# Kernel optimization log

Measured on AMD Instinct MI355X. Metric: run time of the kernel, lower is better.

The kernel has to match this reference:

```python
import jax, jax.numpy as jnp
import numpy as np

B, SX, SY, D = 32, 2048, 2048, 160

def setup_inputs() -> dict:
    key = jax.random.key(0)
    ks = jax.random.split(key, 5)
    s = 1.0 / np.sqrt(D)
    return {
        "x": jax.random.normal(ks[0], (B, SX, D), dtype=jnp.float32),
        "y": jax.random.normal(ks[1], (B, SY, D), dtype=jnp.float32),
        "Wq": jax.random.normal(ks[2], (D, D), dtype=jnp.float32) * s,
        "bq": jnp.zeros((D,), dtype=jnp.float32),
        "Wk": jax.random.normal(ks[3], (D, D), dtype=jnp.float32) * s,
        "bk": jnp.zeros((D,), dtype=jnp.float32),
        "Wv": jax.random.normal(ks[4], (D, D), dtype=jnp.float32) * s,
        "bv": jnp.zeros((D,), dtype=jnp.float32),
    }

def reference(x, y, Wq, bq, Wk, bk, Wv, bv):
    # torch nn.Linear: out = in @ W.T + b, W is [out_dim, in_dim]
    q = jnp.einsum('bxd,ed->bxe', x, Wq) + bq          # [B,SX,D]
    k = jnp.einsum('byd,ed->bye', y, Wk) + bk          # [B,SY,D]
    v = jnp.einsum('byd,ed->bye', y, Wv) + bv          # [B,SY,D]
    scores = jnp.einsum('bxd,byd->bxy', q, k)          # [B,SX,SY] (no scaling in source)
    attn = jax.nn.softmax(scores, axis=-1)
    out = jnp.einsum('bxy,byd->bxd', attn, v)          # dropout is identity at eval
    return out + x                                     # residual
```

## Files before the change

### kernel.cpp

```cpp
#include <hip/hip_runtime.h>

#define LOG2E 1.44269504088896340736f

typedef _Float16 f16;
typedef __attribute__((ext_vector_type(2))) _Float16 f16x2;
typedef __attribute__((ext_vector_type(2))) __fp16 fp16x2;
typedef __attribute__((ext_vector_type(4))) _Float16 f16x4;
typedef __attribute__((ext_vector_type(8))) _Float16 f16x8;
typedef __attribute__((ext_vector_type(4))) float f32x4;
typedef __attribute__((ext_vector_type(16))) float f32x16;
typedef __attribute__((ext_vector_type(8))) unsigned short us8;
typedef __attribute__((ext_vector_type(2))) int i32x2;

#define BB 32
#define SSX 2048
#define SSY 2048
#define DD 160
#define M_TOTAL (BB*SSX)

#define PRS 168
#define VTRS 136
#define RS 168
#define KVB 32
#define VRS 40

__device__ __forceinline__ f32x4 mfma16(f16x8 a, f16x8 b, f32x4 c) {
  return __builtin_amdgcn_mfma_f32_16x16x32_f16(a, b, c, 0, 0, 0);
}

__device__ __forceinline__ f32x16 mfma32(f16x8 a, f16x8 b, f32x16 c) {
  return __builtin_amdgcn_mfma_f32_32x32x16_f16(a, b, c, 0, 0, 0);
}

__device__ __forceinline__ unsigned pk2rtz(float a, float b) {
  union { fp16x2 h; unsigned u; } x;
  x.h = __builtin_amdgcn_cvt_pkrtz(a, b);
  return x.u;
}

__global__ __launch_bounds__(256) void wcvt_kernel(
    const float* __restrict__ Wq, const float* __restrict__ Wk, const float* __restrict__ Wv,
    f16* __restrict__ Wf)
{
  int idx = blockIdx.x*256 + threadIdx.x;
  int which = idx / 6400;
  int off   = idx % 6400;
  const float* src = (which == 0) ? Wq : (which == 1 ? Wk : Wv);
  float4 v = *(const float4*)&src[off*4];
  f16x4 h = { (f16)v.x, (f16)v.y, (f16)v.z, (f16)v.w };
  *(f16x4*)&Wf[which*25600 + off*4] = h;
}

__global__ __launch_bounds__(256, 3) void proj_kernel(
    const float* __restrict__ x, const float* __restrict__ y,
    const float* __restrict__ bq, const float* __restrict__ bk, const float* __restrict__ bv,
    const f16* __restrict__ Wf,
    f16* __restrict__ Qw, f16* __restrict__ Kw, f16* __restrict__ Vtw)
{
  __shared__ __align__(16) f16 buf[160*PRS];
  const int t = threadIdx.x;
  const int wave = t >> 6;
  const int lane = t & 63;
  const int quad = lane >> 4;
  const int l16  = lane & 15;
  const int bid  = (blockIdx.x & 7) * 192 + (blockIdx.x >> 3);
  const int kind = bid % 3;
  const int tile = bid / 3;
  const int row0 = tile * 128;
  const float* src  = (kind == 0) ? x  : y;
  const f16*   W    = Wf + kind*25600;
  const float* bias = (kind == 0) ? bq : (kind == 1 ? bk : bv);

  #pragma unroll
  for (int i = 0; i < 12; ++i) {
    int idx = t + i*256;
    int r = idx / 20, g = idx % 20;
    *(us8*)&buf[r*PRS + g*8] = *(const us8*)&W[idx*8];
  }
  if (t < 128) {
    int idx = t + 3072;
    int r = idx / 20, g = idx % 20;
    *(us8*)&buf[r*PRS + g*8] = *(const us8*)&W[idx*8];
  }

  f16x8 afr0[5], afr1[5];
  {
    const float* r0p = src + (size_t)(row0 + wave*32 + l16)*DD;
    const float* r1p = r0p + 16*DD;
    #pragma unroll
    for (int ks = 0; ks < 5; ++ks) {
      float4 a = *(const float4*)&r0p[ks*32 + quad*8];
      float4 b = *(const float4*)&r0p[ks*32 + quad*8 + 4];
      afr0[ks] = (f16x8){(f16)a.x,(f16)a.y,(f16)a.z,(f16)a.w,
                         (f16)b.x,(f16)b.y,(f16)b.z,(f16)b.w};
      float4 c = *(const float4*)&r1p[ks*32 + quad*8];
      float4 d = *(const float4*)&r1p[ks*32 + quad*8 + 4];
      afr1[ks] = (f16x8){(f16)c.x,(f16)c.y,(f16)c.z,(f16)c.w,
                         (f16)d.x,(f16)d.y,(f16)d.z,(f16)d.w};
    }
  }
  __syncthreads();

  f32x4 acc0[10], acc1[10];
  #pragma unroll
  for (int nt = 0; nt < 10; ++nt) {
    float bs = bias[nt*16 + l16];
    acc0[nt] = (f32x4){bs,bs,bs,bs};
    acc1[nt] = (f32x4){bs,bs,bs,bs};
    #pragma unroll
    for (int ks = 0; ks < 5; ++ks) {
      f16x8 bfr = *(const f16x8*)&buf[(nt*16 + l16)*PRS + ks*32 + quad*8];
      acc0[nt] = mfma16(afr0[ks], bfr, acc0[nt]);
      acc1[nt] = mfma16(afr1[ks], bfr, acc1[nt]);
    }
  }
  __syncthreads();

  if (kind < 2) {
    f16* dst = (kind == 0) ? Qw : Kw;
    #pragma unroll
    for (int nt = 0; nt < 10; ++nt)
      #pragma unroll
      for (int r = 0; r < 4; ++r) {
        buf[(wave*32 + quad*4 + r)*PRS + nt*16 + l16]      = (f16)acc0[nt][r];
        buf[(wave*32 + 16 + quad*4 + r)*PRS + nt*16 + l16] = (f16)acc1[nt][r];
      }
    __syncthreads();
    for (int i = 0; i < 10; ++i) {
      int idx = t + i*256;
      int r = idx / 20, g = idx % 20;
      *(us8*)&dst[(size_t)(row0 + r)*DD + g*8] = *(const us8*)&buf[r*PRS + g*8];
    }
  } else {
    #pragma unroll
    for (int nt = 0; nt < 10; ++nt)
      #pragma unroll
      for (int r = 0; r < 4; ++r) {
        buf[(nt*16 + l16)*VTRS + wave*32 + quad*4 + r]      = (f16)acc0[nt][r];
        buf[(nt*16 + l16)*VTRS + wave*32 + 16 + quad*4 + r] = (f16)acc1[nt][r];
      }
    __syncthreads();
    const int b  = row0 / SSY;
    const int y0 = row0 % SSY;
    for (int i = 0; i < 10; ++i) {
      int idx = t + i*256;
      int d = idx / 16, yg = idx % 16;
      *(us8*)&Vtw[((size_t)b*DD + d)*SSY + y0 + yg*8] = *(const us8*)&buf[d*VTRS + yg*8];
    }
  }
}


#define LOAD_CHUNK(yb) { \
  const f16* ksrc = Kw + ((size_t)b*SSY + (yb))*DD; \
  const f16* vsrc = Vtw + (size_t)b*DD*SSY + (yb); \
  _Pragma("unroll") \
  for (int i = 0; i < 5; ++i) { \
    int idx = t + i*128; int r = idx/20, c = idx%20; \
    kreg[i] = *(const us8*)&ksrc[(size_t)r*DD + c*8]; \
  } \
  _Pragma("unroll") \
  for (int i = 0; i < 5; ++i) { \
    int idx = t + i*128; int d = idx>>2, g = idx&3; \
    vreg[i] = *(const us8*)&vsrc[(size_t)d*SSY + g*8]; \
  } \
}

#define STORE_CHUNK() { \
  _Pragma("unroll") \
  for (int i = 0; i < 5; ++i) { \
    int idx = t + i*128; int r = idx/20, c = idx%20; \
    *(us8*)&K_lds[r*RS + c*8] = kreg[i]; \
  } \
  _Pragma("unroll") \
  for (int i = 0; i < 5; ++i) { \
    int idx = t + i*128; int d = idx>>2, g = idx&3; \
    *(us8*)&Vt_lds[d*VRS + g*8] = vreg[i]; \
  } \
}

__global__ __launch_bounds__(128, 2) void flash_kernel(
    const f16* __restrict__ Qw, const f16* __restrict__ Kw, const f16* __restrict__ Vtw,
    const float* __restrict__ x, float* __restrict__ out)
{
  __shared__ __align__(16) f16 K_lds[KVB*RS];
  __shared__ __align__(16) f16 Vt_lds[160*VRS];
  const int t = threadIdx.x;
  const int wave = t >> 6;
  const int lane = t & 63;
  const int l31  = lane & 31;
  const int hi   = lane >> 5;
  const int bid  = (blockIdx.x & 7) * 128 + (blockIdx.x >> 3);
  const int b    = bid >> 5;
  const int x0   = (bid & 31) * 64;

  us8 kreg[5], vreg[5];
  LOAD_CHUNK(0);

  f16x8 qfr[10];
  #pragma unroll
  for (int h = 0; h < 2; ++h) {
    if (h) __syncthreads();
    const f16* qsrc = Qw + ((size_t)b*SSX + x0 + h*32)*DD;
    for (int i = 0; i < 5; ++i) {
      int idx = t + i*128;
      int r = idx / 20, c = idx % 20;
      *(us8*)&K_lds[r*RS + c*8] = *(const us8*)&qsrc[(size_t)r*DD + c*8];
    }
    __syncthreads();
    if (wave == h) {
      #pragma unroll
      for (int s = 0; s < 10; ++s)
        qfr[s] = *(const f16x8*)&K_lds[l31*RS + s*16 + hi*8];
    }
  }

  f32x16 acc[5];
  #pragma unroll
  for (int i = 0; i < 5; ++i)
    #pragma unroll
    for (int r = 0; r < 16; ++r) acc[i][r] = 0.f;
  float m = -1e30f, l = 0.f;

  for (int yc = 0; yc < SSY/KVB; ++yc) {
    __syncthreads();
    STORE_CHUNK();
    __syncthreads();
    if (yc < SSY/KVB - 1) LOAD_CHUNK((yc+1)*KVB);

    f32x16 S0;
    #pragma unroll
    for (int r = 0; r < 16; ++r) S0[r] = 0.f;
    __builtin_amdgcn_s_setprio(1);
    #pragma unroll
    for (int s = 0; s < 10; ++s) {
      f16x8 k0 = *(const f16x8*)&K_lds[l31*RS + s*16 + hi*8];
      S0 = mfma32(k0, qfr[s], S0);
    }
    __builtin_amdgcn_s_setprio(0);

    float pmax = fmaxf(S0[0], S0[1]);
    #pragma unroll
    for (int r = 2; r < 16; r += 2) pmax = fmaxf(fmaxf(pmax, S0[r]), S0[r+1]);
    pmax = fmaxf(pmax, __shfl_xor(pmax, 32));

    if (__any(pmax > m + 8.f)) {
      float n  = fmaxf(m, pmax);
      float sc = exp2f((m - n)*LOG2E);
      m = n; l *= sc;
      #pragma unroll
      for (int r = 0; r < 16; ++r) {
        float scq = __shfl(sc, (r&3) + 8*(r>>2) + 4*hi);
        #pragma unroll
        for (int dt = 0; dt < 5; ++dt) acc[dt][r] *= scq;
      }
    }

    float lsum = 0.f;
    #pragma unroll
    for (int r = 0; r < 16; ++r) { S0[r] = exp2f((S0[r] - m)*LOG2E); lsum += S0[r]; }
    lsum += __shfl_xor(lsum, 32);
    l += lsum;

    #pragma unroll
    for (int c = 0; c < 2; ++c) {
      const int bo = c*8;
      unsigned L0 = pk2rtz(S0[bo+0], S0[bo+1]), L1 = pk2rtz(S0[bo+2], S0[bo+3]);
      unsigned H0 = pk2rtz(S0[bo+4], S0[bo+5]), H1 = pk2rtz(S0[bo+6], S0[bo+7]);
      i32x2 r02 = __builtin_amdgcn_permlane32_swap((int)L0, (int)H0, false, false);
      i32x2 r13 = __builtin_amdgcn_permlane32_swap((int)L1, (int)H1, false, false);
      union { unsigned u[4]; f16x8 h; } ph;
      ph.u[0] = (unsigned)r02.x; ph.u[1] = (unsigned)r13.x;
      ph.u[2] = (unsigned)r02.y; ph.u[3] = (unsigned)r13.y;
      __builtin_amdgcn_s_setprio(1);
      #pragma unroll
      for (int dt = 0; dt < 5; ++dt) {
        int row = dt*32 + l31;
        f16x8 vf = *(const f16x8*)&Vt_lds[row*VRS + (c*2 + hi)*8];
        acc[dt] = mfma32(ph.h, vf, acc[dt]);
      }
      __builtin_amdgcn_s_setprio(0);
    }
  }

  #pragma unroll
  for (int r = 0; r < 16; ++r) {
    int qr = (r&3) + 8*(r>>2) + 4*hi;
    float rl = 1.f / __shfl(l, qr);
    size_t rowoff = ((size_t)b*SSX + x0 + wave*32 + qr)*DD + l31;
    #pragma unroll
    for (int dt = 0; dt < 5; ++dt) {
      size_t o = rowoff + (size_t)dt*32;
      out[o] = acc[dt][r]*rl + x[o];
    }
  }
}

extern "C" void kernel_launch(void* const* d_in, const int* in_sizes, int n_in,
                              void* d_out, int out_size, void* d_ws, size_t ws_size,
                              hipStream_t stream) {
  const float* x  = (const float*)d_in[0];
  const float* y  = (const float*)d_in[1];
  const float* Wq = (const float*)d_in[2];
  const float* bq = (const float*)d_in[3];
  const float* Wk = (const float*)d_in[4];
  const float* bk = (const float*)d_in[5];
  const float* Wv = (const float*)d_in[6];
  const float* bv = (const float*)d_in[7];

  f16* Qw  = (f16*)d_ws;
  f16* Kw  = Qw + (size_t)M_TOTAL*DD;
  f16* Vtw = Kw + (size_t)M_TOTAL*DD;
  size_t wf_off = (ws_size - 153600) & ~(size_t)255;
  f16* Wf = (f16*)((char*)d_ws + wf_off);

  wcvt_kernel<<<75, 256, 0, stream>>>(Wq, Wk, Wv, Wf);
  proj_kernel<<<1536, 256, 0, stream>>>(x, y, bq, bk, bv, Wf, Qw, Kw, Vtw);
  flash_kernel<<<1024, 128, 0, stream>>>(Qw, Kw, Vtw, x, (float*)d_out);
}
```

Baseline: 272.5 us.

## Double-buffer V tile in LDS and split QK MFMA chain into two accumulators

The V-transpose tile in LDS is now double-buffered. The next chunk's K/V store and the following global load are issued after the QK^T MFMAs and before softmax and PV, so loads overlap compute instead of sitting behind two barriers at the top of each iteration. The QK^T dot is split into two independent accumulator chains to cut MFMA dependency latency, and the max and sum reductions become trees. The projection kernel's launch-bounds occupancy hint drops from 3 to 2, and the extra LDS and registers may lower flash-kernel occupancy.

```diff
diff --git a/kernel.cpp b/kernel.cpp
--- a/kernel.cpp
+++ b/kernel.cpp
@@ -51,7 +51,7 @@
   *(f16x4*)&Wf[which*25600 + off*4] = h;
 }
 
-__global__ __launch_bounds__(256, 3) void proj_kernel(
+__global__ __launch_bounds__(256, 2) void proj_kernel(
     const float* __restrict__ x, const float* __restrict__ y,
     const float* __restrict__ bq, const float* __restrict__ bk, const float* __restrict__ bv,
     const f16* __restrict__ Wf,
@@ -166,7 +166,7 @@
   } \
 }
 
-#define STORE_CHUNK() { \
+#define STORE_CHUNK(vb) { \
   _Pragma("unroll") \
   for (int i = 0; i < 5; ++i) { \
     int idx = t + i*128; int r = idx/20, c = idx%20; \
@@ -175,7 +175,7 @@
   _Pragma("unroll") \
   for (int i = 0; i < 5; ++i) { \
     int idx = t + i*128; int d = idx>>2, g = idx&3; \
-    *(us8*)&Vt_lds[d*VRS + g*8] = vreg[i]; \
+    *(us8*)&Vt_lds[vb][d*VRS + g*8] = vreg[i]; \
   } \
 }
 
@@ -184,7 +184,7 @@
     const float* __restrict__ x, float* __restrict__ out)
 {
   __shared__ __align__(16) f16 K_lds[KVB*RS];
-  __shared__ __align__(16) f16 Vt_lds[160*VRS];
+  __shared__ __align__(16) f16 Vt_lds[2][160*VRS];
   const int t = threadIdx.x;
   const int wave = t >> 6;
   const int lane = t & 63;
@@ -214,6 +214,11 @@
         qfr[s] = *(const f16x8*)&K_lds[l31*RS + s*16 + hi*8];
     }
   }
+  __syncthreads();
+
+  STORE_CHUNK(0);
+  LOAD_CHUNK(KVB);
+  __syncthreads();
 
   f32x16 acc[5];
   #pragma unroll
@@ -223,25 +228,33 @@
   float m = -1e30f, l = 0.f;
 
   for (int yc = 0; yc < SSY/KVB; ++yc) {
-    __syncthreads();
-    STORE_CHUNK();
-    __syncthreads();
-    if (yc < SSY/KVB - 1) LOAD_CHUNK((yc+1)*KVB);
-
-    f32x16 S0;
-    #pragma unroll
-    for (int r = 0; r < 16; ++r) S0[r] = 0.f;
+    const int cur = yc & 1;
+
+    f32x16 Sa, Sb;
+    #pragma unroll
+    for (int r = 0; r < 16; ++r) { Sa[r] = 0.f; Sb[r] = 0.f; }
     __builtin_amdgcn_s_setprio(1);
     #pragma unroll
-    for (int s = 0; s < 10; ++s) {
-      f16x8 k0 = *(const f16x8*)&K_lds[l31*RS + s*16 + hi*8];
-      S0 = mfma32(k0, qfr[s], S0);
+    for (int s = 0; s < 5; ++s) {
+      f16x8 ka = *(const f16x8*)&K_lds[l31*RS + (2*s)*16 + hi*8];
+      f16x8 kb = *(const f16x8*)&K_lds[l31*RS + (2*s+1)*16 + hi*8];
+      Sa = mfma32(ka, qfr[2*s], Sa);
+      Sb = mfma32(kb, qfr[2*s+1], Sb);
     }
     __builtin_amdgcn_s_setprio(0);
-
-    float pmax = fmaxf(S0[0], S0[1]);
-    #pragma unroll
-    for (int r = 2; r < 16; r += 2) pmax = fmaxf(fmaxf(pmax, S0[r]), S0[r+1]);
+    __syncthreads();
+
+    if (yc < SSY/KVB - 1) STORE_CHUNK(cur ^ 1);
+    if (yc < SSY/KVB - 2) LOAD_CHUNK((yc+2)*KVB);
+
+    f32x16 S0 = Sa + Sb;
+
+    float t0 = fmaxf(S0[0], S0[1]),  t1 = fmaxf(S0[2], S0[3]);
+    float t2 = fmaxf(S0[4], S0[5]),  t3 = fmaxf(S0[6], S0[7]);
+    float t4 = fmaxf(S0[8], S0[9]),  t5 = fmaxf(S0[10], S0[11]);
+    float t6 = fmaxf(S0[12], S0[13]), t7 = fmaxf(S0[14], S0[15]);
+    t0 = fmaxf(t0, t1); t2 = fmaxf(t2, t3); t4 = fmaxf(t4, t5); t6 = fmaxf(t6, t7);
+    float pmax = fmaxf(fmaxf(t0, t2), fmaxf(t4, t6));
     pmax = fmaxf(pmax, __shfl_xor(pmax, 32));
 
     if (__any(pmax > m + 8.f)) {
@@ -256,11 +269,16 @@
       }
     }
 
-    float lsum = 0.f;
-    #pragma unroll
-    for (int r = 0; r < 16; ++r) { S0[r] = exp2f((S0[r] - m)*LOG2E); lsum += S0[r]; }
-    lsum += __shfl_xor(lsum, 32);
-    l += lsum;
+    #pragma unroll
+    for (int r = 0; r < 16; ++r) S0[r] = exp2f((S0[r] - m)*LOG2E);
+    {
+      float a0 = S0[0]+S0[1], a1 = S0[2]+S0[3], a2 = S0[4]+S0[5], a3 = S0[6]+S0[7];
+      float a4 = S0[8]+S0[9], a5 = S0[10]+S0[11], a6 = S0[12]+S0[13], a7 = S0[14]+S0[15];
+      a0 += a1; a2 += a3; a4 += a5; a6 += a7;
+      float lsum = (a0 + a2) + (a4 + a6);
+      lsum += __shfl_xor(lsum, 32);
+      l += lsum;
+    }
 
     #pragma unroll
     for (int c = 0; c < 2; ++c) {
@@ -276,11 +294,13 @@
       #pragma unroll
       for (int dt = 0; dt < 5; ++dt) {
         int row = dt*32 + l31;
-        f16x8 vf = *(const f16x8*)&Vt_lds[row*VRS + (c*2 + hi)*8];
+        f16x8 vf = *(const f16x8*)&Vt_lds[cur][row*VRS + (c*2 + hi)*8];
         acc[dt] = mfma32(ph.h, vf, acc[dt]);
       }
       __builtin_amdgcn_s_setprio(0);
     }
+
+    __syncthreads();
   }
 
   #pragma unroll
```

Measured after the change: 289.7 us. 1.06x slower.

## Split KV chunk across wave pairs with 512-thread blocks and merge softmax states

Applied to the files above, without the earlier changes.

Each block now handles 128 query rows with 8 waves. Waves are paired so that each wave of a pair processes half of a 64-row KV chunk, and the two partial online-softmax states (max, sum, accumulator) are merged through LDS at the end. This doubles the KV tile size and halves the number of blocks, amortizing K/V global loads and barriers over more query rows. The cost is an extra cross-wave reduction with several barriers and larger LDS use per block. Each wave's own online-softmax rescaling logic is unchanged.

```diff
diff --git a/kernel.cpp b/kernel.cpp
--- a/kernel.cpp
+++ b/kernel.cpp
@@ -21,8 +21,8 @@
 #define PRS 168
 #define VTRS 136
 #define RS 168
-#define KVB 32
-#define VRS 40
+#define KVB 64
+#define VRS 72
 
 __device__ __forceinline__ f32x4 mfma16(f16x8 a, f16x8 b, f32x4 c) {
   return __builtin_amdgcn_mfma_f32_16x16x32_f16(a, b, c, 0, 0, 0);
@@ -155,63 +155,73 @@
   const f16* ksrc = Kw + ((size_t)b*SSY + (yb))*DD; \
   const f16* vsrc = Vtw + (size_t)b*DD*SSY + (yb); \
   _Pragma("unroll") \
-  for (int i = 0; i < 5; ++i) { \
-    int idx = t + i*128; int r = idx/20, c = idx%20; \
-    kreg[i] = *(const us8*)&ksrc[(size_t)r*DD + c*8]; \
+  for (int i = 0; i < 3; ++i) { \
+    int idx = t + i*512; \
+    if (idx < 1280) { int r = idx/20, c = idx%20; \
+      kreg[i] = *(const us8*)&ksrc[(size_t)r*DD + c*8]; } \
   } \
   _Pragma("unroll") \
-  for (int i = 0; i < 5; ++i) { \
-    int idx = t + i*128; int d = idx>>2, g = idx&3; \
-    vreg[i] = *(const us8*)&vsrc[(size_t)d*SSY + g*8]; \
+  for (int i = 0; i < 3; ++i) { \
+    int idx = t + i*512; \
+    if (idx < 1280) { int d = idx>>3, g = idx&7; \
+      vreg[i] = *(const us8*)&vsrc[(size_t)d*SSY + g*8]; } \
   } \
 }
 
 #define STORE_CHUNK() { \
   _Pragma("unroll") \
-  for (int i = 0; i < 5; ++i) { \
-    int idx = t + i*128; int r = idx/20, c = idx%20; \
-    *(us8*)&K_lds[r*RS + c*8] = kreg[i]; \
+  for (int i = 0; i < 3; ++i) { \
+    int idx = t + i*512; \
+    if (idx < 1280) { int r = idx/20, c = idx%20; \
+      *(us8*)&K_lds[r*RS + c*8] = kreg[i]; } \
   } \
   _Pragma("unroll") \
-  for (int i = 0; i < 5; ++i) { \
-    int idx = t + i*128; int d = idx>>2, g = idx&3; \
-    *(us8*)&Vt_lds[d*VRS + g*8] = vreg[i]; \
+  for (int i = 0; i < 3; ++i) { \
+    int idx = t + i*512; \
+    if (idx < 1280) { int d = idx>>3, g = idx&7; \
+      *(us8*)&Vt_lds[d*VRS + g*8] = vreg[i]; } \
   } \
 }
 
-__global__ __launch_bounds__(128, 2) void flash_kernel(
+__global__ __launch_bounds__(512, 4) void flash_kernel(
     const f16* __restrict__ Qw, const f16* __restrict__ Kw, const f16* __restrict__ Vtw,
     const float* __restrict__ x, float* __restrict__ out)
 {
   __shared__ __align__(16) f16 K_lds[KVB*RS];
   __shared__ __align__(16) f16 Vt_lds[160*VRS];
   const int t = threadIdx.x;
-  const int wave = t >> 6;
+  const int w  = t >> 6;
+  const int wq = w >> 1;
+  const int wk = w & 1;
   const int lane = t & 63;
   const int l31  = lane & 31;
   const int hi   = lane >> 5;
-  const int bid  = (blockIdx.x & 7) * 128 + (blockIdx.x >> 3);
-  const int b    = bid >> 5;
-  const int x0   = (bid & 31) * 64;
-
-  us8 kreg[5], vreg[5];
+  const int bid  = (blockIdx.x & 7) * 64 + (blockIdx.x >> 3);
+  const int b    = bid >> 4;
+  const int x0   = (bid & 15) * 128;
+
+  us8 kreg[3], vreg[3];
   LOAD_CHUNK(0);
 
   f16x8 qfr[10];
   #pragma unroll
   for (int h = 0; h < 2; ++h) {
     if (h) __syncthreads();
-    const f16* qsrc = Qw + ((size_t)b*SSX + x0 + h*32)*DD;
-    for (int i = 0; i < 5; ++i) {
-      int idx = t + i*128;
-      int r = idx / 20, c = idx % 20;
-      *(us8*)&K_lds[r*RS + c*8] = *(const us8*)&qsrc[(size_t)r*DD + c*8];
-    }
-    __syncthreads();
-    if (wave == h) {
+    const f16* qsrc = Qw + ((size_t)b*SSX + x0 + h*64)*DD;
+    #pragma unroll
+    for (int i = 0; i < 3; ++i) {
+      int idx = t + i*512;
+      if (idx < 1280) {
+        int r = idx / 20, c = idx % 20;
+        *(us8*)&K_lds[r*RS + c*8] = *(const us8*)&qsrc[(size_t)r*DD + c*8];
+      }
+    }
+    __syncthreads();
+    if ((wq >> 1) == h) {
+      const int base = (wq & 1)*32;
       #pragma unroll
       for (int s = 0; s < 10; ++s)
-        qfr[s] = *(const f16x8*)&K_lds[l31*RS + s*16 + hi*8];
+        qfr[s] = *(const f16x8*)&K_lds[(base + l31)*RS + s*16 + hi*8];
     }
   }
 
@@ -234,8 +244,8 @@
     __builtin_amdgcn_s_setprio(1);
     #pragma unroll
     for (int s = 0; s < 10; ++s) {
-      f16x8 k0 = *(const f16x8*)&K_lds[l31*RS + s*16 + hi*8];
-      S0 = mfma32(k0, qfr[s], S0);
+      f16x8 kf = *(const f16x8*)&K_lds[(wk*32 + l31)*RS + s*16 + hi*8];
+      S0 = mfma32(kf, qfr[s], S0);
     }
     __builtin_amdgcn_s_setprio(0);
 
@@ -276,22 +286,60 @@
       #pragma unroll
       for (int dt = 0; dt < 5; ++dt) {
         int row = dt*32 + l31;
-        f16x8 vf = *(const f16x8*)&Vt_lds[row*VRS + (c*2 + hi)*8];
+        f16x8 vf = *(const f16x8*)&Vt_lds[row*VRS + wk*32 + (c*2 + hi)*8];
         acc[dt] = mfma32(ph.h, vf, acc[dt]);
       }
       __builtin_amdgcn_s_setprio(0);
     }
   }
 
-  #pragma unroll
-  for (int r = 0; r < 16; ++r) {
-    int qr = (r&3) + 8*(r>>2) + 4*hi;
-    float rl = 1.f / __shfl(l, qr);
-    size_t rowoff = ((size_t)b*SSX + x0 + wave*32 + qr)*DD + l31;
-    #pragma unroll
-    for (int dt = 0; dt < 5; ++dt) {
-      size_t o = rowoff + (size_t)dt*32;
-      out[o] = acc[dt][r]*rl + x[o];
+  __syncthreads();
+  float* ms   = (float*)K_lds;
+  float* ls   = ms + 256;
+  float* accs = (float*)Vt_lds;
+
+  if (hi == 0) ms[w*32 + l31] = m;
+  __syncthreads();
+  float mp    = ms[(wq*2 + (1 - wk))*32 + l31];
+  float mstar = fmaxf(m, mp);
+  float wself = exp2f((m - mstar)*LOG2E);
+  l *= wself;
+  if (hi == 0) ls[w*32 + l31] = l;
+
+  float wsq[16];
+  #pragma unroll
+  for (int r = 0; r < 16; ++r)
+    wsq[r] = __shfl(wself, (r&3) + 8*(r>>2) + 4*hi);
+
+  #pragma unroll
+  for (int dt = 0; dt < 5; ++dt) {
+    if (wk == 1) {
+      #pragma unroll
+      for (int r = 0; r < 16; ++r)
+        accs[(wq*64 + lane)*17 + r] = acc[dt][r] * wsq[r];
+    }
+    __syncthreads();
+    if (wk == 0) {
+      #pragma unroll
+      for (int r = 0; r < 16; ++r)
+        acc[dt][r] = acc[dt][r]*wsq[r] + accs[(wq*64 + lane)*17 + r];
+    }
+    __syncthreads();
+  }
+
+  if (wk == 0) {
+    float lp = ls[(wq*2 + 1)*32 + l31];
+    float lt = l + lp;
+    #pragma unroll
+    for (int r = 0; r < 16; ++r) {
+      int qr = (r&3) + 8*(r>>2) + 4*hi;
+      float rl = 1.f / __shfl(lt, qr);
+      size_t rowoff = ((size_t)b*SSX + x0 + wq*32 + qr)*DD + l31;
+      #pragma unroll
+      for (int dt = 0; dt < 5; ++dt) {
+        size_t o = rowoff + (size_t)dt*32;
+        out[o] = acc[dt][r]*rl + x[o];
+      }
     }
   }
 }
@@ -316,5 +364,5 @@
 
   wcvt_kernel<<<75, 256, 0, stream>>>(Wq, Wk, Wv, Wf);
   proj_kernel<<<1536, 256, 0, stream>>>(x, y, bq, bk, bv, Wf, Qw, Kw, Vtw);
-  flash_kernel<<<1024, 128, 0, stream>>>(Qw, Kw, Vtw, x, (float*)d_out);
-}
+  flash_kernel<<<512, 512, 0, stream>>>(Qw, Kw, Vtw, x, (float*)d_out);
+}
```

Result: slower. 629.1 us (+130.9%).
